# Kernel tuning notes

Measured on AMD Instinct MI355X. Metric: run time of the kernel, lower is better.

## Reference

```python
import jax, jax.numpy as jnp
import numpy as np

HIDDEN = 512
NUM_STEPS = 32
NUM_CLASSES = 97
B, C, H, W = 256, 512, 8, 32


def setup_inputs() -> dict:
    key = jax.random.key(0)
    ks = jax.random.split(key, 16)
    s = 0.02
    inp = {
        "origin_fmap": jax.random.normal(ks[0], (B, C, H, W), jnp.float32),
        "text": jax.random.randint(ks[1], (B, NUM_STEPS), 0, NUM_CLASSES),
        "emb_W": jax.random.normal(ks[2], (HIDDEN, NUM_CLASSES), jnp.float32) * s,
        "emb_b": jnp.zeros((HIDDEN,), jnp.float32),
        "W_ih0": jax.random.normal(ks[3], (4 * HIDDEN, HIDDEN), jnp.float32) * s,
        "W_hh0": jax.random.normal(ks[4], (4 * HIDDEN, HIDDEN), jnp.float32) * s,
        "b_ih0": jnp.zeros((4 * HIDDEN,), jnp.float32),
        "b_hh0": jnp.zeros((4 * HIDDEN,), jnp.float32),
        "W_ih1": jax.random.normal(ks[5], (4 * HIDDEN, HIDDEN), jnp.float32) * s,
        "W_hh1": jax.random.normal(ks[6], (4 * HIDDEN, HIDDEN), jnp.float32) * s,
        "b_ih1": jnp.zeros((4 * HIDDEN,), jnp.float32),
        "b_hh1": jnp.zeros((4 * HIDDEN,), jnp.float32),
        "gen_W": jax.random.normal(ks[7], (NUM_CLASSES, HIDDEN), jnp.float32) * s,
        "gen_b": jnp.zeros((NUM_CLASSES,), jnp.float32),
        "is_train": 1,
    }
    return inp


def _lstm_cell(x, h, c, W_ih, W_hh, b_ih, b_hh):
    # torch LSTM gate order: i, f, g, o
    gates = x @ W_ih.T + h @ W_hh.T + b_ih + b_hh  # [B, 4H]
    i, f, g, o = jnp.split(gates, 4, axis=-1)
    c_new = jax.nn.sigmoid(f) * c + jax.nn.sigmoid(i) * jnp.tanh(g)
    h_new = jax.nn.sigmoid(o) * jnp.tanh(c_new)
    return h_new, c_new


def reference(origin_fmap, text, emb_W, emb_b, W_ih0, W_hh0, b_ih0, b_hh0,
              W_ih1, W_hh1, b_ih1, b_hh1, gen_W, gen_b, is_train):
    b, c, h, w = origin_fmap.shape
    L = h * w
    # [B, L, hidden] - channels == hidden_size by module construction
    fmap = jnp.transpose(origin_fmap, (0, 2, 3, 1)).reshape(b, L, c)
    emb_table = emb_W.T  # one-hot @ emb_W.T == row lookup

    def step(carry, idx_t):
        h0, c0, h1, c1 = carry
        x_emb = emb_table[idx_t] + emb_b          # [B, hidden]
        h0, c0 = _lstm_cell(x_emb, h0, c0, W_ih0, W_hh0, b_ih0, b_hh0)
        h1, c1 = _lstm_cell(h0, h1, c1, W_ih1, W_hh1, b_ih1, b_hh1)
        a = jax.nn.sigmoid(jnp.einsum('bh,blh->bl', h1, fmap))  # [B, L]
        context = jnp.einsum('bl,blh->bh', a, fmap)              # [B, hidden]
        return (h0, c0, h1, c1), (context, a)

    zeros = jnp.zeros((b, c), jnp.float32)
    init = (zeros, zeros, zeros, zeros)
    _, (contexts, attn) = jax.lax.scan(step, init, text.T)  # scan over num_steps
    output_hiddens = jnp.transpose(contexts, (1, 0, 2))       # [B, T, hidden]
    masks = jnp.transpose(attn, (1, 0, 2)).reshape(b, -1, h, w)  # [B, T, H, W]
    g = output_hiddens @ gen_W.T + gen_b                       # [B, T, num_classes]
    return g, output_hiddens, masks
```

## Files before the change

kernel.cpp:

```cpp
#include <hip/hip_runtime.h>

#define B_   256
#define HID  512
#define T_   32
#define L_   256
#define NC   97
#define G4   2048

#define OH_OFF   794624
#define MASK_OFF 4988928

typedef __bf16 v8bf __attribute__((ext_vector_type(8)));
typedef float  v4f  __attribute__((ext_vector_type(4)));
typedef unsigned int v4u __attribute__((ext_vector_type(4)));

__device__ __forceinline__ unsigned short f2bf(float x){
  unsigned u = __float_as_uint(x);
  u += 0x7FFFu + ((u >> 16) & 1u);
  return (unsigned short)(u >> 16);
}
__device__ __forceinline__ float bf2f(unsigned short h){
  return __uint_as_float(((unsigned)h) << 16);
}
__device__ __forceinline__ float sigm(float x){ return 1.f / (1.f + __expf(-x)); }
__device__ __forceinline__ float tanh_f(float x){
  float e = __expf(2.f * x);
  return 1.f - 2.f / (e + 1.f);
}
__device__ __forceinline__ v8bf ld8(const unsigned short* p){
  return *reinterpret_cast<const v8bf*>(p);
}

__global__ void k_wconv(const float* __restrict__ Whh0, const float* __restrict__ Wih1,
                        const float* __restrict__ Whh1, const float* __restrict__ Wih0,
                        unsigned short* __restrict__ Whh0bf, unsigned short* __restrict__ Wcat1bf,
                        unsigned short* __restrict__ Wih0bf){
  int i = blockIdx.x * 256 + threadIdx.x;
  if (i >= G4 * HID) return;
  Whh0bf[i] = f2bf(Whh0[i]);
  Wih0bf[i] = f2bf(Wih0[i]);
  int n = i >> 9, k = i & 511;
  Wcat1bf[(size_t)n * 1024 + k]       = f2bf(Wih1[i]);
  Wcat1bf[(size_t)n * 1024 + 512 + k] = f2bf(Whh1[i]);
}

__global__ void k_small(const float* __restrict__ embW, const float* __restrict__ embb,
                        const float* __restrict__ genW, const float* __restrict__ bih1,
                        const float* __restrict__ bhh1,
                        unsigned short* __restrict__ embXbf, unsigned short* __restrict__ genWbf,
                        float* __restrict__ b1sum){
  int i = blockIdx.x * 256 + threadIdx.x;
  if (i < NC * HID){
    int c = i >> 9, h = i & 511;
    embXbf[i] = f2bf(embW[h * NC + c] + embb[h]);
    genWbf[i] = f2bf(genW[i]);
  }
  if (i < G4) b1sum[i] = bih1[i] + bhh1[i];
}

__global__ void __launch_bounds__(64)
k_embg_m(const unsigned short* __restrict__ embXbf, const unsigned short* __restrict__ Wih0bf,
         const float* __restrict__ bih0, const float* __restrict__ bhh0,
         float* __restrict__ embg){
  int m0 = blockIdx.x * 16, j0 = blockIdx.y * 16;
  int l = threadIdx.x, lr = l & 15, lk = l >> 4;
  int ar = min(m0 + lr, NC - 1);
  v4f acc = {0,0,0,0};
  for (int ks = 0; ks < 16; ++ks){
    int kb = ks * 32 + lk * 8;
    v8bf a  = ld8(embXbf + (size_t)ar * HID + kb);
    v8bf bf = ld8(Wih0bf + (size_t)(j0 + lr) * HID + kb);
    acc = __builtin_amdgcn_mfma_f32_16x16x32_bf16(a, bf, acc, 0, 0, 0);
  }
  int n = j0 + lr;
  float bb = bih0[n] + bhh0[n];
#pragma unroll
  for (int r = 0; r < 4; ++r){
    int c = m0 + lk * 4 + r;
    if (c < NC) embg[(size_t)c * G4 + n] = acc[r] + bb;
  }
}

__global__ void k_fmapT(const float* __restrict__ orig, unsigned short* __restrict__ fT){
  __shared__ float tile[32][33];
  int b = blockIdx.z, c0 = blockIdx.y * 32, l0 = blockIdx.x * 32;
  const float* src = orig + ((size_t)b * HID + c0) * L_ + l0;
  for (int i = 0; i < 32; i += 8)
    tile[threadIdx.y + i][threadIdx.x] = src[(threadIdx.y + i) * L_ + threadIdx.x];
  __syncthreads();
  unsigned short* dst = fT + ((size_t)b * L_ + l0) * HID + c0;
  for (int i = 0; i < 32; i += 8)
    dst[(threadIdx.y + i) * HID + threadIdx.x] = f2bf(tile[threadIdx.x][threadIdx.y + i]);
}

__global__ void __launch_bounds__(256, 4)
k_loop3(const unsigned short* __restrict__ Whh0bf,
        const unsigned short* __restrict__ Wcat1bf,
        const float* __restrict__ embg, const int* __restrict__ text,
        const float* __restrict__ b1sum,
        unsigned short* h0r, unsigned short* h1r,
        unsigned int* flags, unsigned int* rel){
  const int SLOT = B_ * HID;
  const int bid = blockIdx.x;
  const bool isB = bid >= 512;
  const int gb = bid & 511;
  const int band = gb >> 5, jg = gb & 31;
  const int m0 = band * 16, j0 = jg * 16;
  const int tid = threadIdx.x;
  const int w = tid >> 6, l = tid & 63, lr = l & 15, lk = l >> 4;

  __shared__ unsigned short hS[16][1048];
  __shared__ float gbuf[4][16][17];
  __shared__ unsigned tS[16][32];

  unsigned int* relA = rel;
  unsigned int* relB = rel + 16 * 16;

  const int erow = tid >> 4, ecol = tid & 15;
  const int ebrow = m0 + erow, ej = j0 + ecol;
  float creg = 0.f;
  float xb0 = 0.f, xb1 = 0.f, xb2 = 0.f, xb3 = 0.f;
  if (isB){
    xb0 = b1sum[ej]; xb1 = b1sum[512 + ej];
    xb2 = b1sum[1024 + ej]; xb3 = b1sum[1536 + ej];
  } else {
    for (int e = tid; e < 512; e += 256)
      tS[e >> 5][e & 31] = (unsigned)text[(m0 + (e >> 5)) * T_ + (e & 31)] * G4;
  }
  const unsigned short* W = isB ? Wcat1bf : Whh0bf;
  const int wstr = isB ? 1024 : 512;
  const unsigned short* wrow = W + (size_t)(w * HID + j0 + lr) * wstr;

  v8bf wreg[16];
  if (!isB){
#pragma unroll
    for (int i = 0; i < 16; ++i) wreg[i] = ld8(wrow + i * 32 + lk * 8);
  } else {
#pragma unroll
    for (int i = 8; i < 16; ++i) wreg[i] = ld8(wrow + (16 + i) * 32 + lk * 8);
  }

  if (!isB){
    for (int p = 0; p < 32; ++p){
      if (p >= 1){
        if (tid == 0){
          unsigned it = 0;
          while (__hip_atomic_load(&relA[band * 16], __ATOMIC_RELAXED,
                                   __HIP_MEMORY_SCOPE_AGENT) < (unsigned)p){
            if (++it > 1000000u) break;
            __builtin_amdgcn_s_sleep(1);
          }
        }
        __syncthreads();
        asm volatile("" ::: "memory");
      }
      const unsigned short* hA = h0r + (size_t)p * SLOT;
#pragma unroll
      for (int i = 0; i < 4; ++i){
        int e = tid + 256 * i;
        int row = e >> 6, c8 = (e & 63) * 8;
        *(v4u*)&hS[row][c8] = *(const v4u*)(hA + (size_t)(m0 + row) * HID + c8);
      }
      __syncthreads();
      v4f acc = {0,0,0,0};
#pragma unroll
      for (int ks = 0; ks < 16; ++ks){
        v8bf a = *(const v8bf*)&hS[lr][ks * 32 + lk * 8];
        acc = __builtin_amdgcn_mfma_f32_16x16x32_bf16(a, wreg[ks], acc, 0, 0, 0);
      }
#pragma unroll
      for (int r = 0; r < 4; ++r)
        gbuf[w][lk * 4 + r][lr] = acc[r];
      __syncthreads();
      {
        const float* eg = embg + (size_t)tS[erow][p] + ej;
        float xi = eg[0], xf = eg[512], xg = eg[1024], xo = eg[1536];
        float ig = gbuf[0][erow][ecol] + xi, fg = gbuf[1][erow][ecol] + xf;
        float gg = gbuf[2][erow][ecol] + xg, og = gbuf[3][erow][ecol] + xo;
        float cn = sigm(fg) * creg + sigm(ig) * tanh_f(gg);
        creg = cn;
        float hn = sigm(og) * tanh_f(cn);
        unsigned short* hout = h0r + (size_t)(p + 1) * SLOT;
        unsigned v = f2bf(hn);
        unsigned pv = (unsigned)__shfl_xor((int)v, 1);
        if (!(tid & 1)){
          unsigned pack = (v & 0xFFFFu) | (pv << 16);
          __hip_atomic_store((unsigned*)(hout + (size_t)ebrow * HID + ej), pack,
                             __ATOMIC_RELAXED, __HIP_MEMORY_SCOPE_AGENT);
        }
      }
      __syncthreads();
      if (tid == 0)
        __hip_atomic_store(&flags[bid * 16], (unsigned)(p + 1),
                           __ATOMIC_RELAXED, __HIP_MEMORY_SCOPE_AGENT);
      if (jg == 0){
        if (tid < 32){
          const unsigned* fp = &flags[(band * 32 + tid) * 16];
          unsigned it = 0;
          while (__hip_atomic_load(fp, __ATOMIC_RELAXED,
                                   __HIP_MEMORY_SCOPE_AGENT) < (unsigned)(p + 1)){
            if (++it > 1000000u) break;
            __builtin_amdgcn_s_sleep(1);
          }
        }
        __syncthreads();
        if (tid == 0)
          __hip_atomic_store(&relA[band * 16], (unsigned)(p + 1),
                             __ATOMIC_RELAXED, __HIP_MEMORY_SCOPE_AGENT);
      }
    }
  } else {
    for (int p = 1; p <= 32; ++p){
      if (tid == 0){
        unsigned it = 0;
        while (__hip_atomic_load(&relA[band * 16], __ATOMIC_RELAXED,
                                 __HIP_MEMORY_SCOPE_AGENT) < (unsigned)p){
          if (++it > 1000000u) break;
          __builtin_amdgcn_s_sleep(1);
        }
        it = 0;
        while (__hip_atomic_load(&relB[band * 16], __ATOMIC_RELAXED,
                                 __HIP_MEMORY_SCOPE_AGENT) < (unsigned)(p - 1)){
          if (++it > 1000000u) break;
          __builtin_amdgcn_s_sleep(1);
        }
      }
      __syncthreads();
      asm volatile("" ::: "memory");
      const unsigned short* hA = h0r + (size_t)p * SLOT;
      const unsigned short* hB = h1r + (size_t)(p - 1) * SLOT;
#pragma unroll
      for (int i = 0; i < 8; ++i){
        int e = tid + 256 * i;
        int part = e >> 10, ei = e & 1023;
        int row = ei >> 6, c8 = (ei & 63) * 8;
        const unsigned short* src = (part ? hB : hA) + (size_t)(m0 + row) * HID + c8;
        *(v4u*)&hS[row][part * 512 + c8] = *(const v4u*)src;
      }
      __syncthreads();
      v4f acc = {0,0,0,0};
#pragma unroll
      for (int ks = 0; ks < 24; ++ks){
        v8bf bf = ld8(wrow + ks * 32 + lk * 8);
        v8bf a  = *(const v8bf*)&hS[lr][ks * 32 + lk * 8];
        acc = __builtin_amdgcn_mfma_f32_16x16x32_bf16(a, bf, acc, 0, 0, 0);
      }
#pragma unroll
      for (int i = 8; i < 16; ++i){
        v8bf a = *(const v8bf*)&hS[lr][(16 + i) * 32 + lk * 8];
        acc = __builtin_amdgcn_mfma_f32_16x16x32_bf16(a, wreg[i], acc, 0, 0, 0);
      }
#pragma unroll
      for (int r = 0; r < 4; ++r)
        gbuf[w][lk * 4 + r][lr] = acc[r];
      __syncthreads();
      {
        float ig = gbuf[0][erow][ecol] + xb0, fg = gbuf[1][erow][ecol] + xb1;
        float gg = gbuf[2][erow][ecol] + xb2, og = gbuf[3][erow][ecol] + xb3;
        float cn = sigm(fg) * creg + sigm(ig) * tanh_f(gg);
        creg = cn;
        float hn = sigm(og) * tanh_f(cn);
        unsigned short* hout = h1r + (size_t)p * SLOT;
        unsigned v = f2bf(hn);
        unsigned pv = (unsigned)__shfl_xor((int)v, 1);
        if (!(tid & 1)){
          unsigned pack = (v & 0xFFFFu) | (pv << 16);
          __hip_atomic_store((unsigned*)(hout + (size_t)ebrow * HID + ej), pack,
                             __ATOMIC_RELAXED, __HIP_MEMORY_SCOPE_AGENT);
        }
      }
      __syncthreads();
      if (tid == 0)
        __hip_atomic_store(&flags[bid * 16], (unsigned)p,
                           __ATOMIC_RELAXED, __HIP_MEMORY_SCOPE_AGENT);
      if (jg == 0){
        if (tid < 32){
          const unsigned* fp = &flags[(512 + band * 32 + tid) * 16];
          unsigned it = 0;
          while (__hip_atomic_load(fp, __ATOMIC_RELAXED,
                                   __HIP_MEMORY_SCOPE_AGENT) < (unsigned)p){
            if (++it > 1000000u) break;
            __builtin_amdgcn_s_sleep(1);
          }
        }
        __syncthreads();
        if (tid == 0)
          __hip_atomic_store(&relB[band * 16], (unsigned)p,
                             __ATOMIC_RELAXED, __HIP_MEMORY_SCOPE_AGENT);
      }
    }
  }
}

__global__ void __launch_bounds__(256)
k_step2(const unsigned short* __restrict__ Whh0bf,
        const unsigned short* __restrict__ Wcat1bf,
        const float* __restrict__ embg, const int* __restrict__ text,
        const float* __restrict__ b1sum,
        unsigned short* __restrict__ h0r, unsigned short* __restrict__ h1r,
        float* __restrict__ c0, float* __restrict__ c1, int p){
  const int SLOT = B_ * HID;
  const int bid = blockIdx.x;
  const bool isB = bid >= 512;
  if (isB ? (p < 1) : (p >= 32)) return;
  const int gb = bid & 511;
  const int band = gb >> 5, jg = gb & 31;
  const int m0 = band * 16, j0 = jg * 16;
  const int tid = threadIdx.x;
  const int w = tid >> 6, l = tid & 63, lr = l & 15, lk = l >> 4;
  const int t = isB ? (p - 1) : p;

  __shared__ unsigned short hS[16][1048];
  __shared__ float gbuf[4][16][17];

  const unsigned short* hA = h0r + (size_t)p * SLOT;
  const unsigned short* hB = h1r + (size_t)(isB ? (p - 1) : 0) * SLOT;

  if (isB){
#pragma unroll
    for (int i = 0; i < 8; ++i){
      int e = tid + 256 * i;
      int part = e >> 10, ei = e & 1023;
      int row = ei >> 6, c8 = (ei & 63) * 8;
      const unsigned short* src = (part ? hB : hA) + (size_t)(m0 + row) * HID + c8;
      *(v4u*)&hS[row][part * 512 + c8] = *(const v4u*)src;
    }
  } else {
#pragma unroll
    for (int i = 0; i < 4; ++i){
      int e = tid + 256 * i;
      int row = e >> 6, c8 = (e & 63) * 8;
      *(v4u*)&hS[row][c8] = *(const v4u*)(hA + (size_t)(m0 + row) * HID + c8);
    }
  }
  __syncthreads();

  const unsigned short* W = isB ? Wcat1bf : Whh0bf;
  const int wstr = isB ? 1024 : 512;
  const int KS   = isB ? 32 : 16;
  const unsigned short* wrow = W + (size_t)(w * HID + j0 + lr) * wstr;
  v4f acc = {0,0,0,0};
#pragma unroll 4
  for (int ks = 0; ks < KS; ++ks){
    const int kb = ks * 32 + lk * 8;
    v8bf a  = *(const v8bf*)&hS[lr][kb];
    v8bf bf = ld8(wrow + kb);
    acc = __builtin_amdgcn_mfma_f32_16x16x32_bf16(a, bf, acc, 0, 0, 0);
  }
#pragma unroll
  for (int r = 0; r < 4; ++r)
    gbuf[w][lk * 4 + r][lr] = acc[r];
  __syncthreads();

  {
    const int row = tid >> 4, col = tid & 15;
    const int brow = m0 + row, j = j0 + col;
    float xi, xf, xg, xo;
    if (!isB){
      const float* eg = embg + (size_t)text[brow * T_ + t] * G4 + j;
      xi = eg[0]; xf = eg[512]; xg = eg[1024]; xo = eg[1536];
    } else {
      xi = b1sum[j]; xf = b1sum[512 + j];
      xg = b1sum[1024 + j]; xo = b1sum[1536 + j];
    }
    float ig = gbuf[0][row][col] + xi, fg = gbuf[1][row][col] + xf;
    float gg = gbuf[2][row][col] + xg, og = gbuf[3][row][col] + xo;
    float* cst = isB ? c1 : c0;
    size_t ci = (size_t)brow * HID + j;
    float cn = sigm(fg) * cst[ci] + sigm(ig) * tanh_f(gg);
    cst[ci] = cn;
    float hn = sigm(og) * tanh_f(cn);
    unsigned short* hout = isB ? (h1r + (size_t)p * SLOT)
                               : (h0r + (size_t)(p + 1) * SLOT);
    unsigned v = f2bf(hn);
    unsigned pv = (unsigned)__shfl_xor((int)v, 1);
    if (!(tid & 1)){
      unsigned pack = (v & 0xFFFFu) | (pv << 16);
      *(unsigned*)(hout + (size_t)brow * HID + j) = pack;
    }
  }
}

__global__ void __launch_bounds__(256)
k_attn1(const unsigned short* __restrict__ fT, const unsigned short* __restrict__ h1r,
        float* __restrict__ d_out){
  int b = blockIdx.x, tid = threadIdx.x, w = tid >> 6, l = tid & 63;
  int lr = l & 15, lk = l >> 4;
  const unsigned short* fb = fT + (size_t)b * L_ * HID;
  v4f acc[2][4] = {};
  for (int ks = 0; ks < 16; ++ks){
    int kb = ks * 32 + lk * 8;
    v8bf a0 = ld8(h1r + ((size_t)(lr + 1)  * B_ + b) * HID + kb);
    v8bf a1 = ld8(h1r + ((size_t)(lr + 17) * B_ + b) * HID + kb);
#pragma unroll
    for (int fn = 0; fn < 4; ++fn){
      v8bf bf = ld8(fb + (size_t)(w * 64 + fn * 16 + lr) * HID + kb);
      acc[0][fn] = __builtin_amdgcn_mfma_f32_16x16x32_bf16(a0, bf, acc[0][fn], 0, 0, 0);
      acc[1][fn] = __builtin_amdgcn_mfma_f32_16x16x32_bf16(a1, bf, acc[1][fn], 0, 0, 0);
    }
  }
#pragma unroll
  for (int fm = 0; fm < 2; ++fm)
#pragma unroll
    for (int fn = 0; fn < 4; ++fn)
#pragma unroll
      for (int r = 0; r < 4; ++r){
        int tt = fm * 16 + lk * 4 + r;
        int li = w * 64 + fn * 16 + lr;
        d_out[MASK_OFF + ((size_t)b * T_ + tt) * L_ + li] = sigm(acc[fm][fn][r]);
      }
}

__global__ void __launch_bounds__(512)
k_attn2(const unsigned short* __restrict__ fT, const float* __restrict__ d_out_ro,
        float* __restrict__ d_out, unsigned short* __restrict__ ctxbf){
  int b = blockIdx.x, tid = threadIdx.x, w = tid >> 6, l = tid & 63;
  __shared__ float aS[T_][L_];
  const float* ab = d_out_ro + MASK_OFF + (size_t)b * T_ * L_;
  for (int i = tid * 4; i < T_ * L_; i += 512 * 4){
    float4 v = *(const float4*)(ab + i);
    int tt = i >> 8, ll = i & 255;
    aS[tt][ll+0] = v.x; aS[tt][ll+1] = v.y; aS[tt][ll+2] = v.z; aS[tt][ll+3] = v.w;
  }
  __syncthreads();
  float acc[4][8] = {};
  const unsigned short* fb = fT + (size_t)b * L_ * HID + l * 8;
  for (int li = 0; li < L_; ++li){
    ushort4 u0 = *(const ushort4*)(fb + (size_t)li * HID);
    ushort4 u1 = *(const ushort4*)(fb + (size_t)li * HID + 4);
    float f[8] = {bf2f(u0.x), bf2f(u0.y), bf2f(u0.z), bf2f(u0.w),
                  bf2f(u1.x), bf2f(u1.y), bf2f(u1.z), bf2f(u1.w)};
#pragma unroll
    for (int tt = 0; tt < 4; ++tt){
      float a = aS[w * 4 + tt][li];
#pragma unroll
      for (int k = 0; k < 8; ++k) acc[tt][k] += a * f[k];
    }
  }
#pragma unroll
  for (int tt = 0; tt < 4; ++tt)
#pragma unroll
    for (int k = 0; k < 8; ++k){
      size_t o = ((size_t)b * T_ + w * 4 + tt) * HID + l * 8 + k;
      d_out[OH_OFF + o] = acc[tt][k];
      ctxbf[o] = f2bf(acc[tt][k]);
    }
}

__global__ void __launch_bounds__(256)
k_gen_m(const unsigned short* __restrict__ ctxbf, const unsigned short* __restrict__ genWbf,
        const float* __restrict__ genb, float* __restrict__ g){
  int m0 = blockIdx.x * 64 + (threadIdx.x >> 6) * 16;
  int j0 = blockIdx.y * 16;
  int l = threadIdx.x & 63, lr = l & 15, lk = l >> 4;
  int n = j0 + lr, nr = min(n, NC - 1);
  v4f acc = {0,0,0,0};
  for (int ks = 0; ks < 16; ++ks){
    int kb = ks * 32 + lk * 8;
    v8bf a  = ld8(ctxbf + (size_t)(m0 + lr) * HID + kb);
    v8bf bf = ld8(genWbf + (size_t)nr * HID + kb);
    acc = __builtin_amdgcn_mfma_f32_16x16x32_bf16(a, bf, acc, 0, 0, 0);
  }
  if (n < NC){
    float bb = genb[n];
#pragma unroll
    for (int r = 0; r < 4; ++r)
      g[(size_t)(m0 + lk * 4 + r) * NC + n] = acc[r] + bb;
  }
}

__global__ void __launch_bounds__(256)
k_attn_direct(const float* __restrict__ orig, const unsigned short* __restrict__ h1b,
              float* __restrict__ d_out, int t){
  int b = blockIdx.x, tid = threadIdx.x;
  __shared__ float h1s[HID];
  __shared__ float as[L_];
  h1s[tid]       = bf2f(h1b[(size_t)b * HID + tid]);
  h1s[256 + tid] = bf2f(h1b[(size_t)b * HID + 256 + tid]);
  __syncthreads();
  const float* fb = orig + (size_t)b * HID * L_;
  float dot = 0.f;
  for (int ch = 0; ch < HID; ++ch) dot += h1s[ch] * fb[(size_t)ch * L_ + tid];
  float a = sigm(dot);
  as[tid] = a;
  d_out[MASK_OFF + ((size_t)b * T_ + t) * L_ + tid] = a;
  __syncthreads();
  for (int cc = 0; cc < 2; ++cc){
    int ch = tid + cc * 256;
    float s = 0.f;
    for (int ll = 0; ll < L_; ++ll) s += as[ll] * fb[(size_t)ch * L_ + ll];
    d_out[OH_OFF + ((size_t)b * T_ + t) * HID + ch] = s;
  }
}

__global__ void k_gen_v(const float* __restrict__ ctx, const float* __restrict__ genW,
                        const float* __restrict__ genb, float* __restrict__ g){
  int o = blockIdx.x * 256 + threadIdx.x;
  if (o >= B_ * T_ * NC) return;
  int m = o / NC, n = o - m * NC;
  const float4* a = (const float4*)(ctx + (size_t)m * HID);
  const float4* wv = (const float4*)(genW + (size_t)n * HID);
  float s = genb[n];
  for (int k = 0; k < HID / 4; ++k){
    float4 av = a[k], w = wv[k];
    s += av.x * w.x + av.y * w.y + av.z * w.z + av.w * w.w;
  }
  g[o] = s;
}

extern "C" void kernel_launch(void* const* d_in, const int* in_sizes, int n_in,
                              void* d_out, int out_size, void* d_ws, size_t ws_size,
                              hipStream_t stream){
  const float* orig = (const float*)d_in[0];
  const int*   text = (const int*)  d_in[1];
  const float* embW = (const float*)d_in[2];
  const float* embb = (const float*)d_in[3];
  const float* Wih0 = (const float*)d_in[4];
  const float* Whh0 = (const float*)d_in[5];
  const float* bih0 = (const float*)d_in[6];
  const float* bhh0 = (const float*)d_in[7];
  const float* Wih1 = (const float*)d_in[8];
  const float* Whh1 = (const float*)d_in[9];
  const float* bih1 = (const float*)d_in[10];
  const float* bhh1 = (const float*)d_in[11];
  const float* genW = (const float*)d_in[12];
  const float* genb = (const float*)d_in[13];
  float* out = (float*)d_out;

  const size_t SLOTB = (size_t)B_ * HID * 2;

  char* p = (char*)d_ws;
  float* embg  = (float*)p;           p += (size_t)NC * G4 * 4;
  float* b1sum = (float*)p;           p += (size_t)G4 * 4;
  float* c0 = (float*)p;                       p += (size_t)B_ * HID * 4;
  float* c1 = (float*)p;                       p += (size_t)B_ * HID * 4;
  unsigned int* flags = (unsigned int*)p;      p += 1024 * 64;
  unsigned int* rel   = (unsigned int*)p;      p += 32 * 64;
  size_t zbytes = (size_t)((char*)p - (char*)c0);
  unsigned short* Whh0bf  = (unsigned short*)p; p += (size_t)G4 * 512 * 2;
  unsigned short* Wcat1bf = (unsigned short*)p; p += (size_t)G4 * 1024 * 2;
  unsigned short* Wih0bf  = (unsigned short*)p; p += (size_t)G4 * 512 * 2;
  unsigned short* embXbf  = (unsigned short*)p; p += (size_t)NC * HID * 2;
  unsigned short* genWbf  = (unsigned short*)p; p += (size_t)NC * HID * 2;
  unsigned short* h0r = (unsigned short*)p;    p += 34 * SLOTB;
  unsigned short* h1r = (unsigned short*)p;    p += 33 * SLOTB;
  unsigned short* ctxbf = (unsigned short*)p;  p += (size_t)B_ * T_ * HID * 2;
  unsigned short* fmapT = (unsigned short*)p;  p += (size_t)B_ * L_ * HID * 2;
  bool big = ws_size >= (size_t)(p - (char*)d_ws);

  hipMemsetAsync(c0, 0, zbytes, stream);
  hipMemsetAsync(h0r, 0, SLOTB, stream);
  hipMemsetAsync(h1r, 0, SLOTB, stream);

  k_wconv<<<(G4 * HID + 255) / 256, 256, 0, stream>>>(Whh0, Wih1, Whh1, Wih0,
                                                      Whh0bf, Wcat1bf, Wih0bf);
  k_small<<<(NC * HID + 255) / 256, 256, 0, stream>>>(embW, embb, genW, bih1, bhh1,
                                                      embXbf, genWbf, b1sum);
  k_embg_m<<<dim3(7, G4 / 16), 64, 0, stream>>>(embXbf, Wih0bf, bih0, bhh0, embg);
  if (big) k_fmapT<<<dim3(L_ / 32, HID / 32, B_), dim3(32, 8), 0, stream>>>(orig, fmapT);

  hipError_t ce = hipErrorUnknown;
  if (big){
    const unsigned short* a0 = Whh0bf; const unsigned short* a1 = Wcat1bf;
    const float* a2 = embg; const int* a3 = text; const float* a4 = b1sum;
    unsigned short* a5 = h0r; unsigned short* a6 = h1r;
    unsigned int* a7 = flags; unsigned int* a8 = rel;
    void* args[] = {&a0, &a1, &a2, &a3, &a4, &a5, &a6, &a7, &a8};
    ce = hipLaunchCooperativeKernel((const void*)k_loop3, dim3(1024), dim3(256),
                                    args, 0, stream);
  }
  if (ce != hipSuccess){
    for (int pp = 0; pp <= 32; ++pp)
      k_step2<<<1024, 256, 0, stream>>>(Whh0bf, Wcat1bf, embg, text, b1sum,
                                        h0r, h1r, c0, c1, pp);
  }

  if (big){
    k_attn1<<<B_, 256, 0, stream>>>(fmapT, h1r, out);
    k_attn2<<<B_, 512, 0, stream>>>(fmapT, (const float*)out, out, ctxbf);
    k_gen_m<<<dim3(B_ * T_ / 64, 7), 256, 0, stream>>>(ctxbf, genWbf, genb, out);
  } else {
    for (int t = 0; t < T_; ++t)
      k_attn_direct<<<B_, 256, 0, stream>>>(orig, h1r + (size_t)(t + 1) * B_ * HID,
                                            out, t);
    k_gen_v<<<(B_ * T_ * NC + 255) / 256, 256, 0, stream>>>(out + OH_OFF, genW, genb, out);
  }
}
```

Measured before the change: 441.7 us.

## Replace two-level relay barrier with direct flag polling and fuse attention kernels

In the persistent LSTM loop, each block now polls the 32 per-block flags of its band directly instead of waiting on a release counter set by a leader block. This removes one relay hop of latency per step, at the cost of more atomic polling traffic. Separately, the two attention kernels are merged into one. Attention scores are computed per 64-column chunk with MFMA, staged in shared memory and immediately used for the context accumulation, so the mask no longer has to be written and re-read from global memory.

```diff
diff --git a/kernel.cpp b/kernel.cpp
--- a/kernel.cpp
+++ b/kernel.cpp
@@ -99,7 +99,7 @@
         const float* __restrict__ embg, const int* __restrict__ text,
         const float* __restrict__ b1sum,
         unsigned short* h0r, unsigned short* h1r,
-        unsigned int* flags, unsigned int* rel){
+        unsigned int* flags){
   const int SLOT = B_ * HID;
   const int bid = blockIdx.x;
   const bool isB = bid >= 512;
@@ -112,9 +112,6 @@
   __shared__ unsigned short hS[16][1048];
   __shared__ float gbuf[4][16][17];
   __shared__ unsigned tS[16][32];
-
-  unsigned int* relA = rel;
-  unsigned int* relB = rel + 16 * 16;
 
   const int erow = tid >> 4, ecol = tid & 15;
   const int ebrow = m0 + erow, ej = j0 + ecol;
@@ -143,11 +140,12 @@
   if (!isB){
     for (int p = 0; p < 32; ++p){
       if (p >= 1){
-        if (tid == 0){
+        if (tid < 32){
+          const unsigned* fp = &flags[(band * 32 + tid) * 16];
           unsigned it = 0;
-          while (__hip_atomic_load(&relA[band * 16], __ATOMIC_RELAXED,
+          while (__hip_atomic_load(fp, __ATOMIC_RELAXED,
                                    __HIP_MEMORY_SCOPE_AGENT) < (unsigned)p){
-            if (++it > 1000000u) break;
+            if (++it > 2000000u) break;
             __builtin_amdgcn_s_sleep(1);
           }
         }
@@ -193,35 +191,23 @@
       if (tid == 0)
         __hip_atomic_store(&flags[bid * 16], (unsigned)(p + 1),
                            __ATOMIC_RELAXED, __HIP_MEMORY_SCOPE_AGENT);
-      if (jg == 0){
-        if (tid < 32){
-          const unsigned* fp = &flags[(band * 32 + tid) * 16];
-          unsigned it = 0;
-          while (__hip_atomic_load(fp, __ATOMIC_RELAXED,
-                                   __HIP_MEMORY_SCOPE_AGENT) < (unsigned)(p + 1)){
-            if (++it > 1000000u) break;
-            __builtin_amdgcn_s_sleep(1);
-          }
-        }
-        __syncthreads();
-        if (tid == 0)
-          __hip_atomic_store(&relA[band * 16], (unsigned)(p + 1),
-                             __ATOMIC_RELAXED, __HIP_MEMORY_SCOPE_AGENT);
-      }
     }
   } else {
     for (int p = 1; p <= 32; ++p){
-      if (tid == 0){
+      if (tid < 32){
+        const unsigned* fp = &flags[(band * 32 + tid) * 16];
         unsigned it = 0;
-        while (__hip_atomic_load(&relA[band * 16], __ATOMIC_RELAXED,
+        while (__hip_atomic_load(fp, __ATOMIC_RELAXED,
                                  __HIP_MEMORY_SCOPE_AGENT) < (unsigned)p){
-          if (++it > 1000000u) break;
+          if (++it > 2000000u) break;
           __builtin_amdgcn_s_sleep(1);
         }
-        it = 0;
-        while (__hip_atomic_load(&relB[band * 16], __ATOMIC_RELAXED,
+      } else if (tid < 64 && p >= 2){
+        const unsigned* fp = &flags[(512 + band * 32 + (tid - 32)) * 16];
+        unsigned it = 0;
+        while (__hip_atomic_load(fp, __ATOMIC_RELAXED,
                                  __HIP_MEMORY_SCOPE_AGENT) < (unsigned)(p - 1)){
-          if (++it > 1000000u) break;
+          if (++it > 2000000u) break;
           __builtin_amdgcn_s_sleep(1);
         }
       }
@@ -271,23 +257,8 @@
       }
       __syncthreads();
       if (tid == 0)
-        __hip_atomic_store(&flags[bid * 16], (unsigned)p,
+        __hip_atomic_store(&flags[(512 + band * 32 + jg) * 16], (unsigned)p,
                            __ATOMIC_RELAXED, __HIP_MEMORY_SCOPE_AGENT);
-      if (jg == 0){
-        if (tid < 32){
-          const unsigned* fp = &flags[(512 + band * 32 + tid) * 16];
-          unsigned it = 0;
-          while (__hip_atomic_load(fp, __ATOMIC_RELAXED,
-                                   __HIP_MEMORY_SCOPE_AGENT) < (unsigned)p){
-            if (++it > 1000000u) break;
-            __builtin_amdgcn_s_sleep(1);
-          }
-        }
-        __syncthreads();
-        if (tid == 0)
-          __hip_atomic_store(&relB[band * 16], (unsigned)p,
-                             __ATOMIC_RELAXED, __HIP_MEMORY_SCOPE_AGENT);
-      }
     }
   }
 }
@@ -381,69 +352,58 @@
   }
 }
 
-__global__ void __launch_bounds__(256)
-k_attn1(const unsigned short* __restrict__ fT, const unsigned short* __restrict__ h1r,
-        float* __restrict__ d_out){
+__global__ void __launch_bounds__(512)
+k_attn(const unsigned short* __restrict__ fT, const unsigned short* __restrict__ h1r,
+       float* __restrict__ d_out, unsigned short* __restrict__ ctxbf){
   int b = blockIdx.x, tid = threadIdx.x, w = tid >> 6, l = tid & 63;
   int lr = l & 15, lk = l >> 4;
+  int mh = w >> 2, nq = w & 3;
+  __shared__ float aS[32][65];
   const unsigned short* fb = fT + (size_t)b * L_ * HID;
-  v4f acc[2][4] = {};
-  for (int ks = 0; ks < 16; ++ks){
-    int kb = ks * 32 + lk * 8;
-    v8bf a0 = ld8(h1r + ((size_t)(lr + 1)  * B_ + b) * HID + kb);
-    v8bf a1 = ld8(h1r + ((size_t)(lr + 17) * B_ + b) * HID + kb);
-#pragma unroll
-    for (int fn = 0; fn < 4; ++fn){
-      v8bf bf = ld8(fb + (size_t)(w * 64 + fn * 16 + lr) * HID + kb);
-      acc[0][fn] = __builtin_amdgcn_mfma_f32_16x16x32_bf16(a0, bf, acc[0][fn], 0, 0, 0);
-      acc[1][fn] = __builtin_amdgcn_mfma_f32_16x16x32_bf16(a1, bf, acc[1][fn], 0, 0, 0);
-    }
-  }
-#pragma unroll
-  for (int fm = 0; fm < 2; ++fm)
-#pragma unroll
-    for (int fn = 0; fn < 4; ++fn)
-#pragma unroll
-      for (int r = 0; r < 4; ++r){
-        int tt = fm * 16 + lk * 4 + r;
-        int li = w * 64 + fn * 16 + lr;
-        d_out[MASK_OFF + ((size_t)b * T_ + tt) * L_ + li] = sigm(acc[fm][fn][r]);
-      }
-}
-
-__global__ void __launch_bounds__(512)
-k_attn2(const unsigned short* __restrict__ fT, const float* __restrict__ d_out_ro,
-        float* __restrict__ d_out, unsigned short* __restrict__ ctxbf){
-  int b = blockIdx.x, tid = threadIdx.x, w = tid >> 6, l = tid & 63;
-  __shared__ float aS[T_][L_];
-  const float* ab = d_out_ro + MASK_OFF + (size_t)b * T_ * L_;
-  for (int i = tid * 4; i < T_ * L_; i += 512 * 4){
-    float4 v = *(const float4*)(ab + i);
-    int tt = i >> 8, ll = i & 255;
-    aS[tt][ll+0] = v.x; aS[tt][ll+1] = v.y; aS[tt][ll+2] = v.z; aS[tt][ll+3] = v.w;
-  }
-  __syncthreads();
-  float acc[4][8] = {};
-  const unsigned short* fb = fT + (size_t)b * L_ * HID + l * 8;
-  for (int li = 0; li < L_; ++li){
-    ushort4 u0 = *(const ushort4*)(fb + (size_t)li * HID);
-    ushort4 u1 = *(const ushort4*)(fb + (size_t)li * HID + 4);
-    float f[8] = {bf2f(u0.x), bf2f(u0.y), bf2f(u0.z), bf2f(u0.w),
-                  bf2f(u1.x), bf2f(u1.y), bf2f(u1.z), bf2f(u1.w)};
-#pragma unroll
-    for (int tt = 0; tt < 4; ++tt){
-      float a = aS[w * 4 + tt][li];
-#pragma unroll
-      for (int k = 0; k < 8; ++k) acc[tt][k] += a * f[k];
-    }
+  v8bf afr[16];
+#pragma unroll
+  for (int ks = 0; ks < 16; ++ks)
+    afr[ks] = ld8(h1r + ((size_t)(mh * 16 + lr + 1) * B_ + b) * HID + ks * 32 + lk * 8);
+  float vacc[4][8] = {};
+  for (int it = 0; it < 4; ++it){
+    v4f acc = {0,0,0,0};
+#pragma unroll
+    for (int ks = 0; ks < 16; ++ks){
+      v8bf bf = ld8(fb + (size_t)(it * 64 + nq * 16 + lr) * HID + ks * 32 + lk * 8);
+      acc = __builtin_amdgcn_mfma_f32_16x16x32_bf16(afr[ks], bf, acc, 0, 0, 0);
+    }
+#pragma unroll
+    for (int r = 0; r < 4; ++r){
+      int tt = mh * 16 + lk * 4 + r;
+      int li = nq * 16 + lr;
+      float aa = sigm(acc[r]);
+      d_out[MASK_OFF + ((size_t)b * T_ + tt) * L_ + it * 64 + li] = aa;
+      aS[tt][li] = aa;
+    }
+    __syncthreads();
+#pragma unroll 4
+    for (int li = 0; li < 64; ++li){
+      const unsigned short* fr = fb + (size_t)(it * 64 + li) * HID + l * 8;
+      ushort4 u0 = *(const ushort4*)fr;
+      ushort4 u1 = *(const ushort4*)(fr + 4);
+      float f[8] = {bf2f(u0.x), bf2f(u0.y), bf2f(u0.z), bf2f(u0.w),
+                    bf2f(u1.x), bf2f(u1.y), bf2f(u1.z), bf2f(u1.w)};
+#pragma unroll
+      for (int tt = 0; tt < 4; ++tt){
+        float a = aS[w * 4 + tt][li];
+#pragma unroll
+        for (int k = 0; k < 8; ++k) vacc[tt][k] += a * f[k];
+      }
+    }
+    __syncthreads();
   }
 #pragma unroll
   for (int tt = 0; tt < 4; ++tt)
 #pragma unroll
     for (int k = 0; k < 8; ++k){
       size_t o = ((size_t)b * T_ + w * 4 + tt) * HID + l * 8 + k;
-      d_out[OH_OFF + o] = acc[tt][k];
-      ctxbf[o] = f2bf(acc[tt][k]);
+      d_out[OH_OFF + o] = vacc[tt][k];
+      ctxbf[o] = f2bf(vacc[tt][k]);
     }
 }
 
@@ -535,7 +495,6 @@
   float* c0 = (float*)p;                       p += (size_t)B_ * HID * 4;
   float* c1 = (float*)p;                       p += (size_t)B_ * HID * 4;
   unsigned int* flags = (unsigned int*)p;      p += 1024 * 64;
-  unsigned int* rel   = (unsigned int*)p;      p += 32 * 64;
   size_t zbytes = (size_t)((char*)p - (char*)c0);
   unsigned short* Whh0bf  = (unsigned short*)p; p += (size_t)G4 * 512 * 2;
   unsigned short* Wcat1bf = (unsigned short*)p; p += (size_t)G4 * 1024 * 2;
@@ -564,8 +523,8 @@
     const unsigned short* a0 = Whh0bf; const unsigned short* a1 = Wcat1bf;
     const float* a2 = embg; const int* a3 = text; const float* a4 = b1sum;
     unsigned short* a5 = h0r; unsigned short* a6 = h1r;
-    unsigned int* a7 = flags; unsigned int* a8 = rel;
-    void* args[] = {&a0, &a1, &a2, &a3, &a4, &a5, &a6, &a7, &a8};
+    unsigned int* a7 = flags;
+    void* args[] = {&a0, &a1, &a2, &a3, &a4, &a5, &a6, &a7};
     ce = hipLaunchCooperativeKernel((const void*)k_loop3, dim3(1024), dim3(256),
                                     args, 0, stream);
   }
@@ -576,8 +535,7 @@
   }
 
   if (big){
-    k_attn1<<<B_, 256, 0, stream>>>(fmapT, h1r, out);
-    k_attn2<<<B_, 512, 0, stream>>>(fmapT, (const float*)out, out, ctxbf);
+    k_attn<<<B_, 512, 0, stream>>>(fmapT, h1r, out, ctxbf);
     k_gen_m<<<dim3(B_ * T_ / 64, 7), 256, 0, stream>>>(ctxbf, genWbf, genb, out);
   } else {
     for (int t = 0; t < T_; ++t)
```

New measurement: 450.7 us. 1.02x slower.

## Replace two-level release barriers with direct per-block flag polling and split layer-1 GEMM

Applied to the files above, without the earlier changes.

Removes the leader-block (jg==0) aggregation and release counters. Every block now polls the 32 per-block flags of its band directly, which cuts one hop of cross-block latency per step. Layer-1 blocks start the W_ih1·h0 half of the GEMM as soon as h0 is ready, and only then wait for the previous h1 before doing the recurrent half. All 16 recurrent-weight fragments are held in registers. The costs are more global polling traffic (32 lanes per block instead of one) and higher register pressure from the larger wreg set, which may reduce occupancy.

```diff
diff --git a/kernel.cpp b/kernel.cpp
--- a/kernel.cpp
+++ b/kernel.cpp
@@ -99,7 +99,7 @@
         const float* __restrict__ embg, const int* __restrict__ text,
         const float* __restrict__ b1sum,
         unsigned short* h0r, unsigned short* h1r,
-        unsigned int* flags, unsigned int* rel){
+        unsigned int* flags){
   const int SLOT = B_ * HID;
   const int bid = blockIdx.x;
   const bool isB = bid >= 512;
@@ -112,9 +112,6 @@
   __shared__ unsigned short hS[16][1048];
   __shared__ float gbuf[4][16][17];
   __shared__ unsigned tS[16][32];
-
-  unsigned int* relA = rel;
-  unsigned int* relB = rel + 16 * 16;
 
   const int erow = tid >> 4, ecol = tid & 15;
   const int ebrow = m0 + erow, ej = j0 + ecol;
@@ -137,17 +134,18 @@
     for (int i = 0; i < 16; ++i) wreg[i] = ld8(wrow + i * 32 + lk * 8);
   } else {
 #pragma unroll
-    for (int i = 8; i < 16; ++i) wreg[i] = ld8(wrow + (16 + i) * 32 + lk * 8);
+    for (int i = 0; i < 16; ++i) wreg[i] = ld8(wrow + (16 + i) * 32 + lk * 8);
   }
 
   if (!isB){
     for (int p = 0; p < 32; ++p){
       if (p >= 1){
-        if (tid == 0){
+        if (tid < 32){
+          const unsigned* fp = &flags[(band * 32 + tid) * 16];
           unsigned it = 0;
-          while (__hip_atomic_load(&relA[band * 16], __ATOMIC_RELAXED,
+          while (__hip_atomic_load(fp, __ATOMIC_RELAXED,
                                    __HIP_MEMORY_SCOPE_AGENT) < (unsigned)p){
-            if (++it > 1000000u) break;
+            if (++it > 2000000u) break;
             __builtin_amdgcn_s_sleep(1);
           }
         }
@@ -193,60 +191,58 @@
       if (tid == 0)
         __hip_atomic_store(&flags[bid * 16], (unsigned)(p + 1),
                            __ATOMIC_RELAXED, __HIP_MEMORY_SCOPE_AGENT);
-      if (jg == 0){
+    }
+  } else {
+    for (int p = 1; p <= 32; ++p){
+      if (tid < 32){
+        const unsigned* fp = &flags[(band * 32 + tid) * 16];
+        unsigned it = 0;
+        while (__hip_atomic_load(fp, __ATOMIC_RELAXED,
+                                 __HIP_MEMORY_SCOPE_AGENT) < (unsigned)p){
+          if (++it > 2000000u) break;
+          __builtin_amdgcn_s_sleep(1);
+        }
+      }
+      __syncthreads();
+      asm volatile("" ::: "memory");
+      const unsigned short* hA = h0r + (size_t)p * SLOT;
+#pragma unroll
+      for (int i = 0; i < 4; ++i){
+        int e = tid + 256 * i;
+        int row = e >> 6, c8 = (e & 63) * 8;
+        *(v4u*)&hS[row][c8] = *(const v4u*)(hA + (size_t)(m0 + row) * HID + c8);
+      }
+      __syncthreads();
+      v4f acc = {0,0,0,0};
+#pragma unroll
+      for (int ks = 0; ks < 16; ++ks){
+        v8bf bf = ld8(wrow + ks * 32 + lk * 8);
+        v8bf a  = *(const v8bf*)&hS[lr][ks * 32 + lk * 8];
+        acc = __builtin_amdgcn_mfma_f32_16x16x32_bf16(a, bf, acc, 0, 0, 0);
+      }
+      if (p >= 2){
         if (tid < 32){
-          const unsigned* fp = &flags[(band * 32 + tid) * 16];
+          const unsigned* fp = &flags[(512 + band * 32 + tid) * 16];
           unsigned it = 0;
           while (__hip_atomic_load(fp, __ATOMIC_RELAXED,
-                                   __HIP_MEMORY_SCOPE_AGENT) < (unsigned)(p + 1)){
-            if (++it > 1000000u) break;
+                                   __HIP_MEMORY_SCOPE_AGENT) < (unsigned)(p - 1)){
+            if (++it > 2000000u) break;
             __builtin_amdgcn_s_sleep(1);
           }
         }
-        __syncthreads();
-        if (tid == 0)
-          __hip_atomic_store(&relA[band * 16], (unsigned)(p + 1),
-                             __ATOMIC_RELAXED, __HIP_MEMORY_SCOPE_AGENT);
-      }
-    }
-  } else {
-    for (int p = 1; p <= 32; ++p){
-      if (tid == 0){
-        unsigned it = 0;
-        while (__hip_atomic_load(&relA[band * 16], __ATOMIC_RELAXED,
-                                 __HIP_MEMORY_SCOPE_AGENT) < (unsigned)p){
-          if (++it > 1000000u) break;
-          __builtin_amdgcn_s_sleep(1);
-        }
-        it = 0;
-        while (__hip_atomic_load(&relB[band * 16], __ATOMIC_RELAXED,
-                                 __HIP_MEMORY_SCOPE_AGENT) < (unsigned)(p - 1)){
-          if (++it > 1000000u) break;
-          __builtin_amdgcn_s_sleep(1);
-        }
       }
       __syncthreads();
       asm volatile("" ::: "memory");
-      const unsigned short* hA = h0r + (size_t)p * SLOT;
       const unsigned short* hB = h1r + (size_t)(p - 1) * SLOT;
 #pragma unroll
-      for (int i = 0; i < 8; ++i){
+      for (int i = 0; i < 4; ++i){
         int e = tid + 256 * i;
-        int part = e >> 10, ei = e & 1023;
-        int row = ei >> 6, c8 = (ei & 63) * 8;
-        const unsigned short* src = (part ? hB : hA) + (size_t)(m0 + row) * HID + c8;
-        *(v4u*)&hS[row][part * 512 + c8] = *(const v4u*)src;
-      }
-      __syncthreads();
-      v4f acc = {0,0,0,0};
-#pragma unroll
-      for (int ks = 0; ks < 24; ++ks){
-        v8bf bf = ld8(wrow + ks * 32 + lk * 8);
-        v8bf a  = *(const v8bf*)&hS[lr][ks * 32 + lk * 8];
-        acc = __builtin_amdgcn_mfma_f32_16x16x32_bf16(a, bf, acc, 0, 0, 0);
-      }
-#pragma unroll
-      for (int i = 8; i < 16; ++i){
+        int row = e >> 6, c8 = (e & 63) * 8;
+        *(v4u*)&hS[row][512 + c8] = *(const v4u*)(hB + (size_t)(m0 + row) * HID + c8);
+      }
+      __syncthreads();
+#pragma unroll
+      for (int i = 0; i < 16; ++i){
         v8bf a = *(const v8bf*)&hS[lr][(16 + i) * 32 + lk * 8];
         acc = __builtin_amdgcn_mfma_f32_16x16x32_bf16(a, wreg[i], acc, 0, 0, 0);
       }
@@ -271,23 +267,8 @@
       }
       __syncthreads();
       if (tid == 0)
-        __hip_atomic_store(&flags[bid * 16], (unsigned)p,
+        __hip_atomic_store(&flags[(512 + band * 32 + jg) * 16], (unsigned)p,
                            __ATOMIC_RELAXED, __HIP_MEMORY_SCOPE_AGENT);
-      if (jg == 0){
-        if (tid < 32){
-          const unsigned* fp = &flags[(512 + band * 32 + tid) * 16];
-          unsigned it = 0;
-          while (__hip_atomic_load(fp, __ATOMIC_RELAXED,
-                                   __HIP_MEMORY_SCOPE_AGENT) < (unsigned)p){
-            if (++it > 1000000u) break;
-            __builtin_amdgcn_s_sleep(1);
-          }
-        }
-        __syncthreads();
-        if (tid == 0)
-          __hip_atomic_store(&relB[band * 16], (unsigned)p,
-                             __ATOMIC_RELAXED, __HIP_MEMORY_SCOPE_AGENT);
-      }
     }
   }
 }
@@ -535,7 +516,6 @@
   float* c0 = (float*)p;                       p += (size_t)B_ * HID * 4;
   float* c1 = (float*)p;                       p += (size_t)B_ * HID * 4;
   unsigned int* flags = (unsigned int*)p;      p += 1024 * 64;
-  unsigned int* rel   = (unsigned int*)p;      p += 32 * 64;
   size_t zbytes = (size_t)((char*)p - (char*)c0);
   unsigned short* Whh0bf  = (unsigned short*)p; p += (size_t)G4 * 512 * 2;
   unsigned short* Wcat1bf = (unsigned short*)p; p += (size_t)G4 * 1024 * 2;
@@ -564,8 +544,8 @@
     const unsigned short* a0 = Whh0bf; const unsigned short* a1 = Wcat1bf;
     const float* a2 = embg; const int* a3 = text; const float* a4 = b1sum;
     unsigned short* a5 = h0r; unsigned short* a6 = h1r;
-    unsigned int* a7 = flags; unsigned int* a8 = rel;
-    void* args[] = {&a0, &a1, &a2, &a3, &a4, &a5, &a6, &a7, &a8};
+    unsigned int* a7 = flags;
+    void* args[] = {&a0, &a1, &a2, &a3, &a4, &a5, &a6, &a7};
     ce = hipLaunchCooperativeKernel((const void*)k_loop3, dim3(1024), dim3(256),
                                     args, 0, stream);
   }
```

Measured after the change: 433.5 us. No clear change (-1.9%).
